# Kernel tuning notes

Measured on AMD Instinct MI355X. Metric: run time of the kernel, lower is better.

The kernel has to match this reference:

```python
import jax, jax.numpy as jnp
import numpy as np

# Instant-NGP style multiresolution hash grid config
L = 16                      # n_levels
F = 2                       # n_feat_per_entry
LEVEL_SIZE = 524288         # 2^19 hash entries per level
RES = np.array([16, 22, 30, 42, 58, 80, 111, 154, 212, 294, 406, 561, 776, 1072, 1482, 2048], np.int32)
OFFSETS = (np.arange(L + 1) * LEVEL_SIZE).astype(np.int32)
PRIMES = np.array([1, 2654435761, 805459861], dtype=np.uint32)  # spatial hash primes
# 8 corner offsets of a voxel, (8, 3) in {0,1}
CORNERS = np.array([[(c >> d) & 1 for d in range(3)] for c in range(8)], np.int32)


def setup_inputs() -> dict:
    key = jax.random.key(0)
    k1, k2 = jax.random.split(key)
    B = 1000000
    xyz = jax.random.uniform(k1, (B, 3), dtype=jnp.float32)  # points in [0,1)
    embeddings = jax.random.normal(k2, (int(OFFSETS[-1]), F), dtype=jnp.float32) * 0.01
    return {
        'xyz': xyz,
        'embeddings': embeddings,
        'min_xyz': jnp.zeros((3,), jnp.float32),
        'max_xyz': jnp.ones((3,), jnp.float32),
    }


def _encode(xyz, embeddings, min_xyz, max_xyz):
    B = xyz.shape[0]
    norm = (xyz - min_xyz) / (max_xyz - min_xyz)          # (B, 3) in [0,1] if inside grid
    valid = jnp.all((norm >= 0.0) & (norm <= 1.0), axis=-1)  # (B,)
    corners = jnp.asarray(CORNERS)                        # (8, 3)
    primes = jnp.asarray(PRIMES)
    outs = []
    for l in range(L):  # fixed small loop over levels (different resolution per level)
        r = int(RES[l])
        pos = norm * (r - 1)                              # (B, 3) grid coords
        fi = jnp.clip(jnp.floor(pos).astype(jnp.int32), 0, r - 2)  # (B, 3) base corner
        frac = pos - fi.astype(pos.dtype)                 # (B, 3) trilinear fraction
        c = fi[:, None, :] + corners[None, :, :]          # (B, 8, 3) corner coords
        # trilinear interpolation weights, (B, 8)
        w = jnp.prod(jnp.where(corners[None] == 1, frac[:, None, :], 1.0 - frac[:, None, :]), axis=-1)
        # spatial hash into this level's table slice
        cu = c.astype(jnp.uint32)
        h = (cu[..., 0] * primes[0]) ^ (cu[..., 1] * primes[1]) ^ (cu[..., 2] * primes[2])
        lvl_size = jnp.uint32(int(OFFSETS[l + 1] - OFFSETS[l]))
        idx = (h % lvl_size).astype(jnp.int32) + int(OFFSETS[l])   # (B, 8) global entry ids
        feats = embeddings[idx]                           # (B, 8, F) irregular gather
        outs.append(jnp.sum(w[..., None] * feats, axis=1))  # (B, F)
    out = jnp.stack(outs, axis=1).reshape(B, L * F)       # (B, L*F)
    return jnp.where(valid[:, None], out, jnp.zeros((), out.dtype))


def reference(xyz, embeddings, min_xyz, max_xyz):
    return _encode(xyz, embeddings, min_xyz, max_xyz)
```

## Files before the change

kernel.cpp:

```cpp
#include <hip/hip_runtime.h>
#include <hip/hip_fp16.h>
#include <stdint.h>

#define NLEVELS 16
#define BLOCK 256
#define NPT 2

#define P1 2654435761u
#define P2 805459861u
#define HMASK 0x7FFFFu

__device__ __host__ constexpr int DRES(int l) {
    constexpr int r[6] = {16, 22, 30, 42, 58, 80};
    return r[l];
}
__device__ __host__ constexpr uint32_t DOFF(int l) {
    constexpr uint32_t o[7] = {0, 4096, 14744, 41744, 115832, 310944, 822944};
    return o[l];
}
#define DENSE_ENTRIES 822944u
#define HASH16_ENTRIES (10u << 19)
#define HASH16_BYTES ((size_t)HASH16_ENTRIES * 4)
#define DENSE_BYTES  ((size_t)DENSE_ENTRIES * 4)
#define PREP_TOTAL   (HASH16_ENTRIES + DENSE_ENTRIES)

__global__ __launch_bounds__(BLOCK) void prep_kernel(
    const float* __restrict__ emb,
    uint32_t* __restrict__ tab16,
    uint32_t* __restrict__ dense)
{
    const uint32_t i = blockIdx.x * BLOCK + threadIdx.x;
    if (i < HASH16_ENTRIES) {
        const float2 v = *reinterpret_cast<const float2*>(
            emb + (((size_t)(6u << 19)) + i) * 2);
        __half2 hv = __floats2half2_rn(v.x, v.y);
        __builtin_nontemporal_store(*reinterpret_cast<uint32_t*>(&hv), &tab16[i]);
    } else if (i < PREP_TOTAL) {
        const uint32_t j = i - HASH16_ENTRIES;
        int l = 0;
        #pragma unroll
        for (int q = 1; q < 6; ++q) if (j >= DOFF(q)) l = q;
        const int r = DRES(l);
        const uint32_t rel = j - DOFF(l);
        const int z = rel / (uint32_t)(r * r);
        const uint32_t rem = rel - (uint32_t)z * (uint32_t)(r * r);
        const int y = rem / (uint32_t)r;
        const int x = rem - (uint32_t)y * (uint32_t)r;
        const uint32_t h = ((uint32_t)x ^ ((uint32_t)y * P1) ^ ((uint32_t)z * P2)) & HMASK;
        const float2 v = *reinterpret_cast<const float2*>(
            emb + (((size_t)l << 19) + h) * 2);
        __half2 hv = __floats2half2_rn(v.x, v.y);
        dense[j] = *reinterpret_cast<uint32_t*>(&hv);
    }
}


struct PointCtx { float nx, ny, nz; bool valid; };

__device__ __forceinline__ PointCtx make_ctx(const float* __restrict__ xyz, int pt, int B,
                                             float mn0, float mn1, float mn2,
                                             float inv0, float inv1, float inv2)
{
    PointCtx P;
    P.nx = P.ny = P.nz = 0.0f;
    P.valid = false;
    if (pt < B) {
        const float x = xyz[3 * pt + 0];
        const float y = xyz[3 * pt + 1];
        const float z = xyz[3 * pt + 2];
        P.nx = (x - mn0) * inv0;
        P.ny = (y - mn1) * inv1;
        P.nz = (z - mn2) * inv2;
        P.valid = (P.nx >= 0.0f) && (P.nx <= 1.0f) &&
                  (P.ny >= 0.0f) && (P.ny <= 1.0f) &&
                  (P.nz >= 0.0f) && (P.nz <= 1.0f);
    }
    return P;
}

struct C8 { uint32_t idx[8]; float w[8]; };

__device__ __forceinline__ void frac_setup(const PointCtx& P, int r,
                                           int& fx, int& fy, int& fz,
                                           float& wx0, float& wx1,
                                           float& wy0, float& wy1,
                                           float& wz0, float& wz1)
{
    const float rm1 = (float)(r - 1);
    const float px = P.nx * rm1, py = P.ny * rm1, pz = P.nz * rm1;
    fx = (int)floorf(px); fx = min(max(fx, 0), r - 2);
    fy = (int)floorf(py); fy = min(max(fy, 0), r - 2);
    fz = (int)floorf(pz); fz = min(max(fz, 0), r - 2);
    wx1 = px - (float)fx; wx0 = 1.0f - wx1;
    wy1 = py - (float)fy; wy0 = 1.0f - wy1;
    wz1 = pz - (float)fz; wz0 = 1.0f - wz1;
}

__device__ __forceinline__ C8 mk_hash(const PointCtx& P, int r)
{
    int fx, fy, fz; float wx0, wx1, wy0, wy1, wz0, wz1;
    frac_setup(P, r, fx, fy, fz, wx0, wx1, wy0, wy1, wz0, wz1);
    const uint32_t hx0 = (uint32_t)fx,        hx1 = hx0 + 1u;
    const uint32_t hy0 = (uint32_t)fy * P1,   hy1 = hy0 + P1;
    const uint32_t hz0 = (uint32_t)fz * P2,   hz1 = hz0 + P2;
    C8 c;
    #pragma unroll
    for (int k = 0; k < 8; ++k) {
        c.idx[k] = (((k & 1) ? hx1 : hx0) ^
                    ((k & 2) ? hy1 : hy0) ^
                    ((k & 4) ? hz1 : hz0)) & HMASK;
        c.w[k] = ((k & 1) ? wx1 : wx0) * ((k & 2) ? wy1 : wy0) * ((k & 4) ? wz1 : wz0);
    }
    return c;
}

__device__ __forceinline__ C8 mk_dense(const PointCtx& P, int r, uint32_t off)
{
    int fx, fy, fz; float wx0, wx1, wy0, wy1, wz0, wz1;
    frac_setup(P, r, fx, fy, fz, wx0, wx1, wy0, wy1, wz0, wz1);
    const uint32_t base = off + (uint32_t)(fx + fy * r + fz * r * r);
    C8 c;
    #pragma unroll
    for (int k = 0; k < 8; ++k) {
        c.idx[k] = base + (uint32_t)((k & 1) + ((k & 2) ? r : 0) + ((k & 4) ? r * r : 0));
        c.w[k] = ((k & 1) ? wx1 : wx0) * ((k & 2) ? wy1 : wy0) * ((k & 4) ? wz1 : wz0);
    }
    return c;
}

__device__ __forceinline__ float2 accum8(const C8& c, const uint32_t* e, bool valid)
{
    float a = 0.0f, b = 0.0f;
    #pragma unroll
    for (int k = 0; k < 8; ++k) {
        const float2 f = __half22float2(*reinterpret_cast<const __half2*>(&e[k]));
        a = fmaf(c.w[k], f.x, a);
        b = fmaf(c.w[k], f.y, b);
    }
    float2 o;
    o.x = valid ? a : 0.0f;
    o.y = valid ? b : 0.0f;
    return o;
}

__device__ __forceinline__ void nt_store_f2h(uint32_t* p, float2 v)
{
    __half2 h = __floats2half2_rn(v.x, v.y);
    __builtin_nontemporal_store(*reinterpret_cast<uint32_t*>(&h), p);
}

__global__ __launch_bounds__(BLOCK, 4) void gather_mega_kernel(
    const float* __restrict__ xyz,
    const uint32_t* __restrict__ tab16,
    const uint32_t* __restrict__ dense,
    const float* __restrict__ minv,
    const float* __restrict__ maxv,
    uint32_t* __restrict__ slab,
    int B, int blocks2)
{
    constexpr int HRES[10] = {111, 154, 212, 294, 406, 561, 776, 1072, 1482, 2048};

    const int seg = blockIdx.x / blocks2;
    const int blk = blockIdx.x - seg * blocks2;

    const int t = threadIdx.x;
    const int p0 = blk * (NPT * BLOCK) + t;
    const int p1 = p0 + BLOCK;

    const float mn0 = minv[0], mn1 = minv[1], mn2 = minv[2];
    const float inv0 = 1.0f / (maxv[0] - mn0);
    const float inv1 = 1.0f / (maxv[1] - mn1);
    const float inv2 = 1.0f / (maxv[2] - mn2);

    const PointCtx A  = make_ctx(xyz, p0, B, mn0, mn1, mn2, inv0, inv1, inv2);
    const PointCtx Bc = make_ctx(xyz, p1, B, mn0, mn1, mn2, inv0, inv1, inv2);

    if (seg == 0) {
        #pragma unroll
        for (int l = 0; l < 5; ++l) {
            const C8 c0 = mk_dense(A,  DRES(l), DOFF(l));
            const C8 c1 = mk_dense(Bc, DRES(l), DOFF(l));
            uint32_t e0[8], e1[8];
            #pragma unroll
            for (int k = 0; k < 8; ++k) e0[k] = dense[c0.idx[k]];
            #pragma unroll
            for (int k = 0; k < 8; ++k) e1[k] = dense[c1.idx[k]];
            const float2 o0 = accum8(c0, e0, A.valid);
            const float2 o1 = accum8(c1, e1, Bc.valid);
            if (p0 < B) nt_store_f2h(&slab[(size_t)l * B + p0], o0);
            if (p1 < B) nt_store_f2h(&slab[(size_t)l * B + p1], o1);
        }
    } else if (seg == 1) {
        const C8 c0 = mk_dense(A,  DRES(5), DOFF(5));
        const C8 c1 = mk_dense(Bc, DRES(5), DOFF(5));
        uint32_t e0[8], e1[8];
        #pragma unroll
        for (int k = 0; k < 8; ++k) e0[k] = dense[c0.idx[k]];
        #pragma unroll
        for (int k = 0; k < 8; ++k) e1[k] = dense[c1.idx[k]];
        const float2 o0 = accum8(c0, e0, A.valid);
        const float2 o1 = accum8(c1, e1, Bc.valid);
        if (p0 < B) nt_store_f2h(&slab[(size_t)5 * B + p0], o0);
        if (p1 < B) nt_store_f2h(&slab[(size_t)5 * B + p1], o1);
    } else {
        const int l = seg + 4;
        const int r = HRES[seg - 2];
        const uint32_t* __restrict__ lt = tab16 + ((size_t)(l - 6) << 19);
        const C8 c0 = mk_hash(A,  r);
        const C8 c1 = mk_hash(Bc, r);
        uint32_t e0[8], e1[8];
        #pragma unroll
        for (int k = 0; k < 8; ++k) e0[k] = lt[c0.idx[k]];
        #pragma unroll
        for (int k = 0; k < 8; ++k) e1[k] = lt[c1.idx[k]];
        const float2 o0 = accum8(c0, e0, A.valid);
        const float2 o1 = accum8(c1, e1, Bc.valid);
        if (p0 < B) nt_store_f2h(&slab[(size_t)l * B + p0], o0);
        if (p1 < B) nt_store_f2h(&slab[(size_t)l * B + p1], o1);
    }
}

__global__ __launch_bounds__(BLOCK) void transpose_kernel(
    const uint32_t* __restrict__ slab,
    float* __restrict__ out,
    int B)
{
    __shared__ float s[32][BLOCK + 1];
    const int t = threadIdx.x;
    const int pt = blockIdx.x * BLOCK + t;

    #pragma unroll
    for (int l = 0; l < NLEVELS; ++l) {
        float2 v = make_float2(0.0f, 0.0f);
        if (pt < B) {
            const uint32_t bits = __builtin_nontemporal_load(&slab[(size_t)l * B + pt]);
            v = __half22float2(*reinterpret_cast<const __half2*>(&bits));
        }
        s[2 * l + 0][t] = v.x;
        s[2 * l + 1][t] = v.y;
    }
    __syncthreads();

    const size_t chunk = (size_t)blockIdx.x * (BLOCK * 32);
    const size_t total = (size_t)B * 32;
    #pragma unroll
    for (int k = 0; k < 32; ++k) {
        const int flat = k * BLOCK + t;
        const int p = flat >> 5;
        const int c = flat & 31;
        const size_t g = chunk + (size_t)flat;
        if (g < total) __builtin_nontemporal_store(s[c][p], &out[g]);
    }
}

__global__ __launch_bounds__(BLOCK) void hashgrid_fused_kernel(
    const float* __restrict__ xyz,
    const float* __restrict__ emb,
    const float* __restrict__ minv,
    const float* __restrict__ maxv,
    float* __restrict__ out,
    int B)
{
    constexpr int RES[NLEVELS] = {16, 22, 30, 42, 58, 80, 111, 154,
                                  212, 294, 406, 561, 776, 1072, 1482, 2048};
    __shared__ float s[32][BLOCK + 1];
    const int t = threadIdx.x;
    const int pt = blockIdx.x * BLOCK + t;

    const float mn0 = minv[0], mn1 = minv[1], mn2 = minv[2];
    const float inv0 = 1.0f / (maxv[0] - mn0);
    const float inv1 = 1.0f / (maxv[1] - mn1);
    const float inv2 = 1.0f / (maxv[2] - mn2);

    const PointCtx P = make_ctx(xyz, pt, B, mn0, mn1, mn2, inv0, inv1, inv2);

    #pragma unroll
    for (int l = 0; l < NLEVELS; ++l) {
        const C8 c = mk_hash(P, RES[l]);
        const float* __restrict__ lemb = emb + ((size_t)l << 20);
        float acc0 = 0.0f, acc1 = 0.0f;
        #pragma unroll
        for (int k = 0; k < 8; ++k) {
            const float2 f = *reinterpret_cast<const float2*>(
                lemb + ((size_t)c.idx[k] << 1));
            acc0 = fmaf(c.w[k], f.x, acc0);
            acc1 = fmaf(c.w[k], f.y, acc1);
        }
        s[2 * l + 0][t] = P.valid ? acc0 : 0.0f;
        s[2 * l + 1][t] = P.valid ? acc1 : 0.0f;
    }
    __syncthreads();
    const size_t chunk = (size_t)blockIdx.x * (BLOCK * 32);
    const size_t total = (size_t)B * 32;
    #pragma unroll
    for (int k = 0; k < 32; ++k) {
        const int flat = k * BLOCK + t;
        const int p = flat >> 5;
        const int c = flat & 31;
        const size_t g = chunk + (size_t)flat;
        if (g < total) out[g] = s[c][p];
    }
}

extern "C" void kernel_launch(void* const* d_in, const int* in_sizes, int n_in,
                              void* d_out, int out_size, void* d_ws, size_t ws_size,
                              hipStream_t stream) {
    const float* xyz = (const float*)d_in[0];
    const float* emb = (const float*)d_in[1];
    const float* mn  = (const float*)d_in[2];
    const float* mx  = (const float*)d_in[3];
    float* out = (float*)d_out;

    const int B = in_sizes[0] / 3;
    const int blocks1 = (B + BLOCK - 1) / BLOCK;
    const int blocks2 = (B + NPT * BLOCK - 1) / (NPT * BLOCK);

    const size_t slab_bytes = (size_t)NLEVELS * (size_t)B * 4;
    const size_t ws_needed = slab_bytes + HASH16_BYTES + DENSE_BYTES;

    if (ws_size >= ws_needed) {
        uint32_t* slab  = (uint32_t*)d_ws;
        uint32_t* tab16 = (uint32_t*)((char*)d_ws + slab_bytes);
        uint32_t* dense = (uint32_t*)((char*)d_ws + slab_bytes + HASH16_BYTES);

        hipLaunchKernelGGL(prep_kernel,
                           dim3((PREP_TOTAL + BLOCK - 1) / BLOCK), dim3(BLOCK),
                           0, stream, emb, tab16, dense);

        hipLaunchKernelGGL(gather_mega_kernel, dim3(12 * blocks2), dim3(BLOCK), 0, stream,
                           xyz, tab16, dense, mn, mx, slab, B, blocks2);

        hipLaunchKernelGGL(transpose_kernel, dim3(blocks1), dim3(BLOCK), 0, stream,
                           slab, out, B);
    } else {
        hipLaunchKernelGGL(hashgrid_fused_kernel, dim3(blocks1), dim3(BLOCK), 0, stream,
                           xyz, emb, mn, mx, out, B);
    }
}
```

Before: 313.4 us.

## Pack dense levels as 2x2 corner quads and pair hash fetches

```diff
diff --git a/kernel.cpp b/kernel.cpp
--- a/kernel.cpp
+++ b/kernel.cpp
@@ -14,20 +14,48 @@
     constexpr int r[6] = {16, 22, 30, 42, 58, 80};
     return r[l];
 }
-__device__ __host__ constexpr uint32_t DOFF(int l) {
-    constexpr uint32_t o[7] = {0, 4096, 14744, 41744, 115832, 310944, 822944};
+__device__ __host__ constexpr uint32_t QOFF(int l) {
+    constexpr uint32_t o[7] = {0, 3600, 13302, 38532, 109134, 297576, 796856};
     return o[l];
 }
-#define DENSE_ENTRIES 822944u
+#define QUAD_ENTRIES 796856u
 #define HASH16_ENTRIES (10u << 19)
 #define HASH16_BYTES ((size_t)HASH16_ENTRIES * 4)
-#define DENSE_BYTES  ((size_t)DENSE_ENTRIES * 4)
-#define PREP_TOTAL   (HASH16_ENTRIES + DENSE_ENTRIES)
+#define QUAD_BYTES   ((size_t)QUAD_ENTRIES * 16)
+#define PREP_TOTAL   (HASH16_ENTRIES + QUAD_ENTRIES)
+
+
+__device__ __forceinline__ uint32_t fetch_pack(const float* __restrict__ emb,
+                                               int l, uint32_t x, uint32_t y, uint32_t z)
+{
+    const uint32_t h = (x ^ (y * P1) ^ (z * P2)) & HMASK;
+    const float2 v = *reinterpret_cast<const float2*>(emb + (((size_t)l << 19) + h) * 2);
+    __half2 hv = __floats2half2_rn(v.x, v.y);
+    return *reinterpret_cast<uint32_t*>(&hv);
+}
+
+template <int L>
+__device__ __forceinline__ void qbuild(uint32_t rel, const float* __restrict__ emb,
+                                       uint4* __restrict__ quad)
+{
+    constexpr int r = DRES(L);
+    constexpr int rW = r - 1;
+    const uint32_t fz = rel / (uint32_t)(rW * rW);
+    const uint32_t rem = rel - fz * (uint32_t)(rW * rW);
+    const uint32_t fy = rem / (uint32_t)rW;
+    const uint32_t fx = rem - fy * (uint32_t)rW;
+    uint4 q;
+    q.x = fetch_pack(emb, L, fx,     fy,     fz);
+    q.y = fetch_pack(emb, L, fx + 1, fy,     fz);
+    q.z = fetch_pack(emb, L, fx,     fy + 1, fz);
+    q.w = fetch_pack(emb, L, fx + 1, fy + 1, fz);
+    quad[QOFF(L) + rel] = q;
+}
 
 __global__ __launch_bounds__(BLOCK) void prep_kernel(
     const float* __restrict__ emb,
     uint32_t* __restrict__ tab16,
-    uint32_t* __restrict__ dense)
+    uint4* __restrict__ quad)
 {
     const uint32_t i = blockIdx.x * BLOCK + threadIdx.x;
     if (i < HASH16_ENTRIES) {
@@ -37,20 +65,12 @@
         __builtin_nontemporal_store(*reinterpret_cast<uint32_t*>(&hv), &tab16[i]);
     } else if (i < PREP_TOTAL) {
         const uint32_t j = i - HASH16_ENTRIES;
-        int l = 0;
-        #pragma unroll
-        for (int q = 1; q < 6; ++q) if (j >= DOFF(q)) l = q;
-        const int r = DRES(l);
-        const uint32_t rel = j - DOFF(l);
-        const int z = rel / (uint32_t)(r * r);
-        const uint32_t rem = rel - (uint32_t)z * (uint32_t)(r * r);
-        const int y = rem / (uint32_t)r;
-        const int x = rem - (uint32_t)y * (uint32_t)r;
-        const uint32_t h = ((uint32_t)x ^ ((uint32_t)y * P1) ^ ((uint32_t)z * P2)) & HMASK;
-        const float2 v = *reinterpret_cast<const float2*>(
-            emb + (((size_t)l << 19) + h) * 2);
-        __half2 hv = __floats2half2_rn(v.x, v.y);
-        dense[j] = *reinterpret_cast<uint32_t*>(&hv);
+        if      (j < QOFF(1)) qbuild<0>(j - QOFF(0), emb, quad);
+        else if (j < QOFF(2)) qbuild<1>(j - QOFF(1), emb, quad);
+        else if (j < QOFF(3)) qbuild<2>(j - QOFF(2), emb, quad);
+        else if (j < QOFF(4)) qbuild<3>(j - QOFF(3), emb, quad);
+        else if (j < QOFF(5)) qbuild<4>(j - QOFF(4), emb, quad);
+        else                  qbuild<5>(j - QOFF(5), emb, quad);
     }
 }
 
@@ -78,8 +98,6 @@
     return P;
 }
 
-struct C8 { uint32_t idx[8]; float w[8]; };
-
 __device__ __forceinline__ void frac_setup(const PointCtx& P, int r,
                                            int& fx, int& fy, int& fz,
                                            float& wx0, float& wx1,
@@ -96,50 +114,77 @@
     wz1 = pz - (float)fz; wz0 = 1.0f - wz1;
 }
 
-__device__ __forceinline__ C8 mk_hash(const PointCtx& P, int r)
+__device__ __forceinline__ float2 h2f(uint32_t e)
+{
+    return __half22float2(*reinterpret_cast<const __half2*>(&e));
+}
+
+__device__ __forceinline__ float2 quad_encode(const PointCtx& P, int r, uint32_t qoff,
+                                              const uint4* __restrict__ quad)
 {
     int fx, fy, fz; float wx0, wx1, wy0, wy1, wz0, wz1;
     frac_setup(P, r, fx, fy, fz, wx0, wx1, wy0, wy1, wz0, wz1);
-    const uint32_t hx0 = (uint32_t)fx,        hx1 = hx0 + 1u;
-    const uint32_t hy0 = (uint32_t)fy * P1,   hy1 = hy0 + P1;
-    const uint32_t hz0 = (uint32_t)fz * P2,   hz1 = hz0 + P2;
-    C8 c;
-    #pragma unroll
-    for (int k = 0; k < 8; ++k) {
-        c.idx[k] = (((k & 1) ? hx1 : hx0) ^
-                    ((k & 2) ? hy1 : hy0) ^
-                    ((k & 4) ? hz1 : hz0)) & HMASK;
-        c.w[k] = ((k & 1) ? wx1 : wx0) * ((k & 2) ? wy1 : wy0) * ((k & 4) ? wz1 : wz0);
-    }
-    return c;
-}
-
-__device__ __forceinline__ C8 mk_dense(const PointCtx& P, int r, uint32_t off)
+    const int rW = r - 1;
+    const uint32_t base = qoff + (uint32_t)(fx + fy * rW + fz * rW * rW);
+    const uint4 q0 = quad[base];
+    const uint4 q1 = quad[base + (uint32_t)(rW * rW)];
+
+    const float2 a0 = h2f(q0.x), b0 = h2f(q0.y), c0 = h2f(q0.z), d0 = h2f(q0.w);
+    const float2 a1 = h2f(q1.x), b1 = h2f(q1.y), c1 = h2f(q1.z), d1 = h2f(q1.w);
+
+    const float p0x = wy0 * (wx0 * a0.x + wx1 * b0.x) + wy1 * (wx0 * c0.x + wx1 * d0.x);
+    const float p0y = wy0 * (wx0 * a0.y + wx1 * b0.y) + wy1 * (wx0 * c0.y + wx1 * d0.y);
+    const float p1x = wy0 * (wx0 * a1.x + wx1 * b1.x) + wy1 * (wx0 * c1.x + wx1 * d1.x);
+    const float p1y = wy0 * (wx0 * a1.y + wx1 * b1.y) + wy1 * (wx0 * c1.y + wx1 * d1.y);
+
+    float2 o;
+    o.x = P.valid ? (wz0 * p0x + wz1 * p1x) : 0.0f;
+    o.y = P.valid ? (wz0 * p0y + wz1 * p1y) : 0.0f;
+    return o;
+}
+
+__device__ __forceinline__ float2 hash_encode(const PointCtx& P, int r,
+                                              const uint32_t* __restrict__ lt)
 {
     int fx, fy, fz; float wx0, wx1, wy0, wy1, wz0, wz1;
     frac_setup(P, r, fx, fy, fz, wx0, wx1, wy0, wy1, wz0, wz1);
-    const uint32_t base = off + (uint32_t)(fx + fy * r + fz * r * r);
-    C8 c;
-    #pragma unroll
-    for (int k = 0; k < 8; ++k) {
-        c.idx[k] = base + (uint32_t)((k & 1) + ((k & 2) ? r : 0) + ((k & 4) ? r * r : 0));
-        c.w[k] = ((k & 1) ? wx1 : wx0) * ((k & 2) ? wy1 : wy0) * ((k & 4) ? wz1 : wz0);
-    }
-    return c;
-}
-
-__device__ __forceinline__ float2 accum8(const C8& c, const uint32_t* e, bool valid)
-{
-    float a = 0.0f, b = 0.0f;
-    #pragma unroll
-    for (int k = 0; k < 8; ++k) {
-        const float2 f = __half22float2(*reinterpret_cast<const __half2*>(&e[k]));
-        a = fmaf(c.w[k], f.x, a);
-        b = fmaf(c.w[k], f.y, b);
+    const uint32_t hx0 = (uint32_t)fx;
+    const uint32_t hy0 = (uint32_t)fy * P1, hy1 = hy0 + P1;
+    const uint32_t hz0 = (uint32_t)fz * P2, hz1 = hz0 + P2;
+    const bool oddx = (fx & 1) != 0;
+
+    uint32_t i0[4];
+    uint2 pr[4];
+    #pragma unroll
+    for (int yz = 0; yz < 4; ++yz) {
+        const uint32_t rest = ((yz & 1) ? hy1 : hy0) ^ ((yz & 2) ? hz1 : hz0);
+        i0[yz] = (hx0 ^ rest) & HMASK;
+        pr[yz] = *reinterpret_cast<const uint2*>(lt + (i0[yz] & ~1u));
+    }
+    uint32_t e1x[4] = {0, 0, 0, 0};
+    if (oddx) {
+        #pragma unroll
+        for (int yz = 0; yz < 4; ++yz) {
+            const uint32_t rest = ((yz & 1) ? hy1 : hy0) ^ ((yz & 2) ? hz1 : hz0);
+            e1x[yz] = lt[((hx0 + 1u) ^ rest) & HMASK];
+        }
+    }
+
+    float acc0 = 0.0f, acc1 = 0.0f;
+    #pragma unroll
+    for (int yz = 0; yz < 4; ++yz) {
+        const float wyz = ((yz & 1) ? wy1 : wy0) * ((yz & 2) ? wz1 : wz0);
+        const uint32_t eA = (i0[yz] & 1u) ? pr[yz].y : pr[yz].x;
+        const uint32_t eB0 = (i0[yz] & 1u) ? pr[yz].x : pr[yz].y;
+        const uint32_t eB = oddx ? e1x[yz] : eB0;
+        const float2 cA = h2f(eA);
+        const float2 cB = h2f(eB);
+        acc0 += wyz * (wx0 * cA.x + wx1 * cB.x);
+        acc1 += wyz * (wx0 * cA.y + wx1 * cB.y);
     }
     float2 o;
-    o.x = valid ? a : 0.0f;
-    o.y = valid ? b : 0.0f;
+    o.x = P.valid ? acc0 : 0.0f;
+    o.y = P.valid ? acc1 : 0.0f;
     return o;
 }
 
@@ -152,7 +197,7 @@
 __global__ __launch_bounds__(BLOCK, 4) void gather_mega_kernel(
     const float* __restrict__ xyz,
     const uint32_t* __restrict__ tab16,
-    const uint32_t* __restrict__ dense,
+    const uint4* __restrict__ quad,
     const float* __restrict__ minv,
     const float* __restrict__ maxv,
     uint32_t* __restrict__ slab,
@@ -178,43 +223,22 @@
     if (seg == 0) {
         #pragma unroll
         for (int l = 0; l < 5; ++l) {
-            const C8 c0 = mk_dense(A,  DRES(l), DOFF(l));
-            const C8 c1 = mk_dense(Bc, DRES(l), DOFF(l));
-            uint32_t e0[8], e1[8];
-            #pragma unroll
-            for (int k = 0; k < 8; ++k) e0[k] = dense[c0.idx[k]];
-            #pragma unroll
-            for (int k = 0; k < 8; ++k) e1[k] = dense[c1.idx[k]];
-            const float2 o0 = accum8(c0, e0, A.valid);
-            const float2 o1 = accum8(c1, e1, Bc.valid);
+            const float2 o0 = quad_encode(A,  DRES(l), QOFF(l), quad);
+            const float2 o1 = quad_encode(Bc, DRES(l), QOFF(l), quad);
             if (p0 < B) nt_store_f2h(&slab[(size_t)l * B + p0], o0);
             if (p1 < B) nt_store_f2h(&slab[(size_t)l * B + p1], o1);
         }
     } else if (seg == 1) {
-        const C8 c0 = mk_dense(A,  DRES(5), DOFF(5));
-        const C8 c1 = mk_dense(Bc, DRES(5), DOFF(5));
-        uint32_t e0[8], e1[8];
-        #pragma unroll
-        for (int k = 0; k < 8; ++k) e0[k] = dense[c0.idx[k]];
-        #pragma unroll
-        for (int k = 0; k < 8; ++k) e1[k] = dense[c1.idx[k]];
-        const float2 o0 = accum8(c0, e0, A.valid);
-        const float2 o1 = accum8(c1, e1, Bc.valid);
+        const float2 o0 = quad_encode(A,  DRES(5), QOFF(5), quad);
+        const float2 o1 = quad_encode(Bc, DRES(5), QOFF(5), quad);
         if (p0 < B) nt_store_f2h(&slab[(size_t)5 * B + p0], o0);
         if (p1 < B) nt_store_f2h(&slab[(size_t)5 * B + p1], o1);
     } else {
         const int l = seg + 4;
         const int r = HRES[seg - 2];
         const uint32_t* __restrict__ lt = tab16 + ((size_t)(l - 6) << 19);
-        const C8 c0 = mk_hash(A,  r);
-        const C8 c1 = mk_hash(Bc, r);
-        uint32_t e0[8], e1[8];
-        #pragma unroll
-        for (int k = 0; k < 8; ++k) e0[k] = lt[c0.idx[k]];
-        #pragma unroll
-        for (int k = 0; k < 8; ++k) e1[k] = lt[c1.idx[k]];
-        const float2 o0 = accum8(c0, e0, A.valid);
-        const float2 o1 = accum8(c1, e1, Bc.valid);
+        const float2 o0 = hash_encode(A,  r, lt);
+        const float2 o1 = hash_encode(Bc, r, lt);
         if (p0 < B) nt_store_f2h(&slab[(size_t)l * B + p0], o0);
         if (p1 < B) nt_store_f2h(&slab[(size_t)l * B + p1], o1);
     }
@@ -234,7 +258,7 @@
         float2 v = make_float2(0.0f, 0.0f);
         if (pt < B) {
             const uint32_t bits = __builtin_nontemporal_load(&slab[(size_t)l * B + pt]);
-            v = __half22float2(*reinterpret_cast<const __half2*>(&bits));
+            v = h2f(bits);
         }
         s[2 * l + 0][t] = v.x;
         s[2 * l + 1][t] = v.y;
@@ -276,15 +300,22 @@
 
     #pragma unroll
     for (int l = 0; l < NLEVELS; ++l) {
-        const C8 c = mk_hash(P, RES[l]);
+        int fx, fy, fz; float wx0, wx1, wy0, wy1, wz0, wz1;
+        frac_setup(P, RES[l], fx, fy, fz, wx0, wx1, wy0, wy1, wz0, wz1);
+        const uint32_t hx0 = (uint32_t)fx, hx1 = hx0 + 1u;
+        const uint32_t hy0 = (uint32_t)fy * P1, hy1 = hy0 + P1;
+        const uint32_t hz0 = (uint32_t)fz * P2, hz1 = hz0 + P2;
         const float* __restrict__ lemb = emb + ((size_t)l << 20);
         float acc0 = 0.0f, acc1 = 0.0f;
         #pragma unroll
         for (int k = 0; k < 8; ++k) {
-            const float2 f = *reinterpret_cast<const float2*>(
-                lemb + ((size_t)c.idx[k] << 1));
-            acc0 = fmaf(c.w[k], f.x, acc0);
-            acc1 = fmaf(c.w[k], f.y, acc1);
+            const uint32_t h = (((k & 1) ? hx1 : hx0) ^
+                                ((k & 2) ? hy1 : hy0) ^
+                                ((k & 4) ? hz1 : hz0)) & HMASK;
+            const float2 f = *reinterpret_cast<const float2*>(lemb + ((size_t)h << 1));
+            const float w = ((k & 1) ? wx1 : wx0) * ((k & 2) ? wy1 : wy0) * ((k & 4) ? wz1 : wz0);
+            acc0 = fmaf(w, f.x, acc0);
+            acc1 = fmaf(w, f.y, acc1);
         }
         s[2 * l + 0][t] = P.valid ? acc0 : 0.0f;
         s[2 * l + 1][t] = P.valid ? acc1 : 0.0f;
@@ -316,19 +347,19 @@
     const int blocks2 = (B + NPT * BLOCK - 1) / (NPT * BLOCK);
 
     const size_t slab_bytes = (size_t)NLEVELS * (size_t)B * 4;
-    const size_t ws_needed = slab_bytes + HASH16_BYTES + DENSE_BYTES;
+    const size_t ws_needed = slab_bytes + HASH16_BYTES + QUAD_BYTES;
 
     if (ws_size >= ws_needed) {
         uint32_t* slab  = (uint32_t*)d_ws;
         uint32_t* tab16 = (uint32_t*)((char*)d_ws + slab_bytes);
-        uint32_t* dense = (uint32_t*)((char*)d_ws + slab_bytes + HASH16_BYTES);
+        uint4*    quad  = (uint4*)((char*)d_ws + slab_bytes + HASH16_BYTES);
 
         hipLaunchKernelGGL(prep_kernel,
                            dim3((PREP_TOTAL + BLOCK - 1) / BLOCK), dim3(BLOCK),
-                           0, stream, emb, tab16, dense);
+                           0, stream, emb, tab16, quad);
 
         hipLaunchKernelGGL(gather_mega_kernel, dim3(12 * blocks2), dim3(BLOCK), 0, stream,
-                           xyz, tab16, dense, mn, mx, slab, B, blocks2);
+                           xyz, tab16, quad, mn, mx, slab, B, blocks2);
 
         hipLaunchKernelGGL(transpose_kernel, dim3(blocks1), dim3(BLOCK), 0, stream,
                            slab, out, B);
```

Measured after the change: 368.5 us. +17.6%, slower.
